# Optimization experiments

Measured on AMD Instinct MI355X. Metric: run time of the kernel, lower is better.

Reference implementation:

```python
import jax, jax.numpy as jnp
import numpy as np

T, L, H, C, D_IN, ED, N, E = 4, 3, 1, 256, 20, 10, 4096, 65536
D = H * C  # 256, pooling width
AH = 4     # pooling attention heads


def setup_inputs() -> dict:
    key = jax.random.key(0)
    ks = jax.random.split(key, 24)
    g = lambda k, s, sc=0.05: jax.random.normal(k, s, jnp.float32) * sc
    return {
        "x": jax.random.normal(ks[0], (N, D_IN), jnp.float32),
        "src": jax.random.randint(ks[1], (E,), 0, N),
        "dst": jax.random.randint(ks[2], (E,), 0, N),
        "edge_attr": jax.random.normal(ks[3], (E, ED), jnp.float32),
        "edge_type": jax.random.randint(ks[4], (E,), 0, T),
        # GATConv params per (edge_type, layer)
        "W0": g(ks[5], (T, D_IN, H * C)),          # layer 0 lin
        "W12": g(ks[6], (T, 2, H * C, H * C)),     # layers 1,2 lin
        "att_src": g(ks[7], (T, L, H, C)),
        "att_dst": g(ks[8], (T, L, H, C)),
        "att_edge": g(ks[9], (T, L, H, C)),
        "lin_edge_w": g(ks[10], (T, L, ED, H * C)),
        "biases": g(ks[11], (T, L, C)),            # H=1 so concat/mean both give C
        "edge_type_weights": jnp.ones((T,), jnp.float32) / T,
        # pooling: MultiheadAttention(D, 4 heads)
        "in_proj_w": g(ks[12], (3 * D, D)),
        "in_proj_b": g(ks[13], (3 * D,)),
        "out_proj_w": g(ks[14], (D, D)),
        "out_proj_b": g(ks[15], (D,)),
        # fusion MLP: 3D -> 2D -> 256
        "fus_w1": g(ks[16], (3 * D, 2 * D)),
        "fus_b1": g(ks[17], (2 * D,)),
        "fus_w2": g(ks[18], (2 * D, 256)),
        "fus_b2": g(ks[19], (256,)),
    }


def _gat(h, src, dst, mask, e_attr, W, a_s, a_d, a_e, We, b, concat):
    # PyG GATConv (edge_dim, add_self_loops=True, fill_value='mean'), eval mode
    Nn = h.shape[0]
    Hh, Cc = a_s.shape
    xl = (h @ W).reshape(Nn, Hh, Cc)
    s_src = jnp.sum(xl * a_s, -1)   # [N,H]
    s_dst = jnp.sum(xl * a_d, -1)   # [N,H]
    s_e = jnp.sum((e_attr @ We).reshape(-1, Hh, Cc) * a_e, -1)  # [E,H]
    # self-loop edge_attr = per-node mean of masked incoming edge_attr
    m = mask.astype(h.dtype)
    cnt = jax.ops.segment_sum(m, dst, Nn)
    loop_attr = jax.ops.segment_sum(e_attr * m[:, None], dst, Nn) / jnp.maximum(cnt, 1.0)[:, None]
    s_loop = jnp.sum((loop_attr @ We).reshape(Nn, Hh, Cc) * a_e, -1)  # [N,H]
    a_real = jax.nn.leaky_relu(s_src[src] + s_dst[dst] + s_e, 0.2)
    a_real = jnp.where(mask[:, None], a_real, -1e30)  # mask edges not of this type
    a_loop = jax.nn.leaky_relu(s_src + s_dst + s_loop, 0.2)
    ar = jnp.arange(Nn)
    idx = jnp.concatenate([dst, ar])    # destination of each (edge + self-loop)
    sidx = jnp.concatenate([src, ar])   # source of each
    scores = jnp.concatenate([a_real, a_loop], 0)  # [E+N, H]
    smax = jax.ops.segment_max(scores, idx, Nn)
    ex = jnp.exp(scores - smax[idx])
    ssum = jax.ops.segment_sum(ex, idx, Nn)
    alpha = ex / (ssum[idx] + 1e-16)
    out = jax.ops.segment_sum(xl[sidx] * alpha[:, :, None], idx, Nn)  # [N,H,C]
    out = out.reshape(Nn, Hh * Cc) if concat else out.mean(1)
    return out + b


def reference(x, src, dst, edge_attr, edge_type, W0, W12, att_src, att_dst,
              att_edge, lin_edge_w, biases, edge_type_weights, in_proj_w,
              in_proj_b, out_proj_w, out_proj_b, fus_w1, fus_b1, fus_w2, fus_b2):
    outs = []
    for t in range(T):
        mask = edge_type == t
        h = x
        for i in range(L):
            W = W0[t] if i == 0 else W12[t, i - 1]
            h = _gat(h, src, dst, mask, edge_attr, W, att_src[t, i],
                     att_dst[t, i], att_edge[t, i], lin_edge_w[t, i],
                     biases[t, i], concat=(i < L - 1))
            h = jax.nn.elu(h)  # dropout off in eval
        outs.append(h)
    w = jax.nn.softmax(edge_type_weights)
    h = sum(w[t] * outs[t] for t in range(T))  # [N, D]
    # HierarchicalGraphPooling
    mean_p = h.mean(0)
    max_p = h.max(0)
    qkv = h @ in_proj_w.T + in_proj_b
    q, k, v = jnp.split(qkv, 3, axis=-1)
    HD = D // AH
    q = q.reshape(-1, AH, HD)
    k = k.reshape(-1, AH, HD)
    v = v.reshape(-1, AH, HD)
    att = jax.nn.softmax(jnp.einsum('nhd,mhd->hnm', q, k) / np.float32(np.sqrt(HD)), axis=-1)
    o = jnp.einsum('hnm,mhd->nhd', att, v).reshape(-1, D) @ out_proj_w.T + out_proj_b
    attn_p = o.mean(0)
    comb = jnp.concatenate([mean_p, max_p, attn_p])  # [3D]
    g = jax.nn.relu(comb @ fus_w1 + fus_b1)
    g = jax.nn.relu(g @ fus_w2 + fus_b2)
    return g[None, :]
```

## Files before the change

### kernel.cpp

```cpp
#include <hip/hip_runtime.h>
#include <math.h>

#define T 4
#define LL 3
#define C 256
#define DIN 20
#define NN 4096
#define EE 65536
#define AHD 4
#define MCH 8
#define QKS 72
#define AST 264
#define SLOTN (16384*64)

#define W_CURSOR 0
#define W_SLSRC  16384
#define F_SLSE   (W_SLSRC + SLOTN)
#define F_XL     (F_SLSE + 3*SLOTN)
#define F_H      (F_XL + T*NN*C/2)
#define F_OPART  F_XL
#define F_SSRC   (F_H + T*NN*C/2)
#define F_SDST   (F_SSRC + T*NN)
#define F_WE     (F_SDST + T*NN)
#define F_HACC   (F_WE + 128)
#define F_WT     (F_HACC + NN*C/2)
#define F_QKV    (F_WT + 768*256/2)
#define F_DPART  (F_QKV + NN*768/2)
#define F_MEANP  (F_DPART + MCH*NN*AHD)
#define F_MAXP   (F_MEANP + C)
#define F_OMEAN  (F_MAXP + C)
#define F_ATTNP  (F_OMEAN + C)
#define F_G1     (F_ATTNP + C)
#define U_W12P   (F_G1 + 512)
#define WS_WORDS (U_W12P + 262144)

static __device__ __forceinline__ float lrelu(float x){ return x > 0.f ? x : 0.2f*x; }
static __device__ __forceinline__ float eluf(float x){ return x > 0.f ? x : __expf(x) - 1.f; }

typedef _Float16 half2_t __attribute__((ext_vector_type(2)));
typedef _Float16 v8h __attribute__((ext_vector_type(8)));
typedef float v4f __attribute__((ext_vector_type(4)));

static __device__ __forceinline__ unsigned pk2(float x, float y){
  half2_t h; h.x = (_Float16)x; h.y = (_Float16)y;
  return __builtin_bit_cast(unsigned, h);
}
static __device__ __forceinline__ unsigned pk2h(_Float16 x, _Float16 y){
  half2_t h; h.x = x; h.y = y;
  return __builtin_bit_cast(unsigned, h);
}
static __device__ __forceinline__ float4 up4(uint2 u){
  half2_t a = __builtin_bit_cast(half2_t, u.x);
  half2_t b = __builtin_bit_cast(half2_t, u.y);
  return make_float4((float)a.x, (float)a.y, (float)b.x, (float)b.y);
}
static __device__ __forceinline__ uint2 dn4(float4 v){
  return make_uint2(pk2(v.x, v.y), pk2(v.z, v.w));
}

static __device__ inline void atomicMaxF(float* addr, float val){
  int* ai = (int*)addr;
  int old = __float_as_int(*addr);
  while (__int_as_float(old) < val){
    int assumed = old;
    old = atomicCAS(ai, assumed, __float_as_int(val));
    if (old == assumed) break;
  }
}

__global__ __launch_bounds__(256) void prep_k(
    const float* __restrict__ x, const float* __restrict__ W0,
    const float* __restrict__ attS, const float* __restrict__ attD,
    _Float16* __restrict__ xlo, float* __restrict__ ssrc, float* __restrict__ sdst,
    const float* __restrict__ w12, _Float16* __restrict__ wpT,
    const float* __restrict__ ipw, _Float16* __restrict__ ip16,
    const float* __restrict__ linE, const float* __restrict__ attE,
    float* we, float* fbase, int* cursor){
  __shared__ float smem[64*65];
  __shared__ float red[64];
  int by = blockIdx.y, bx = blockIdx.x, tid = threadIdx.x;
  if (by < 4){
    int t = by;
    const float* W = W0 + (size_t)t*DIN*C;
    int n0 = bx*8;
    for (int j = 0; j < 8; j++)
      for (int k = tid; k < DIN; k += 256)
        smem[j*DIN + k] = x[(n0+j)*DIN + k];
    __syncthreads();
    float acc[8] = {0,0,0,0,0,0,0,0};
    int c = tid;
    for (int k = 0; k < DIN; k += 4){
      float w0 = W[(k+0)*C + c], w1 = W[(k+1)*C + c], w2 = W[(k+2)*C + c], w3 = W[(k+3)*C + c];
      #pragma unroll
      for (int j = 0; j < 8; j++){
        float4 h4 = *(const float4*)&smem[j*DIN + k];
        acc[j] += w0*h4.x + w1*h4.y + w2*h4.z + w3*h4.w;
      }
    }
    #pragma unroll
    for (int j = 0; j < 8; j++) xlo[((size_t)t*NN + n0 + j)*C + c] = (_Float16)acc[j];
    float aS = attS[t*LL*C + c], aD = attD[t*LL*C + c];
    int lane = c & 63, w = c >> 6;
    #pragma unroll
    for (int j = 0; j < 8; j++){
      float v1 = acc[j]*aS, v2 = acc[j]*aD;
      #pragma unroll
      for (int off = 32; off > 0; off >>= 1){ v1 += __shfl_down(v1, off); v2 += __shfl_down(v2, off); }
      if (lane == 0){ red[j*8 + w] = v1; red[j*8 + 4 + w] = v2; }
    }
    __syncthreads();
    if (c < 16){
      int j = c >> 1, which = c & 1;
      const float* r = red + j*8 + which*4;
      float s = r[0] + r[1] + r[2] + r[3];
      (which ? sdst : ssrc)[t*NN + n0 + j] = s;
    }
  } else if (by < 12){
    if (bx < 16){
      int b8 = by - 4;
      int k0 = (bx >> 2)*64, n0 = (bx & 3)*64;
      const float* src = w12 + ((size_t)b8*256 + k0)*256 + n0;
      int row = tid >> 2, l4 = (tid & 3)*4;
      #pragma unroll
      for (int pass = 0; pass < 4; pass++){
        float4 v = *(const float4*)(src + (size_t)row*256 + pass*16 + l4);
        int o = row*65 + pass*16 + l4;
        smem[o+0] = v.x; smem[o+1] = v.y; smem[o+2] = v.z; smem[o+3] = v.w;
      }
      __syncthreads();
      int n = tid >> 2, seg = tid & 3;
      _Float16* dstp = wpT + ((size_t)b8*256 + n0 + n)*256 + k0 + seg*16;
      v8h h0, h1;
      #pragma unroll
      for (int i = 0; i < 8; i++) h0[i] = (_Float16)smem[(seg*16 + i)*65 + n];
      #pragma unroll
      for (int i = 0; i < 8; i++) h1[i] = (_Float16)smem[(seg*16 + 8 + i)*65 + n];
      *(v8h*)(dstp) = h0;
      *(v8h*)(dstp + 8) = h1;
    }
  } else if (by < 15){
    if (bx < 256){
      int j = (by - 12)*256 + bx;
      ip16[(size_t)j*256 + tid] = (_Float16)ipw[(size_t)j*256 + tid];
    }
  } else {
    if (bx < 12){
      int t = bx / 3, l = bx % 3;
      float ae = attE[(t*LL + l)*C + tid];
      const float* lw = linE + (size_t)((t*LL + l)*10)*C;
      for (int k = 0; k < 10; k++) smem[k*C + tid] = lw[k*C + tid]*ae;
      __syncthreads();
      if (tid < 10){
        float s = 0.f;
        for (int i = 0; i < C; i++) s += smem[tid*C + i];
        we[(t*LL + l)*10 + tid] = s;
      }
    } else if (bx == 12){
      fbase[tid] = 0.f;
      fbase[256 + tid] = -1e30f;
      fbase[512 + tid] = 0.f;
    } else if (bx >= 64 && bx < 128){
      cursor[(bx - 64)*256 + tid] = 0;
    }
  }
}

__global__ __launch_bounds__(256) void scat_k(const int* __restrict__ dst, const int* __restrict__ ety,
                                              const int* __restrict__ srcv, const float* __restrict__ eattr,
                                              const float* __restrict__ we,
                                              int* cursor, int* slot_src, float* slot_se){
  int e = blockIdx.x*256 + threadIdx.x;
  if (e < EE){
    int t = ety[e];
    int gid = dst[e]*T + t;
    int p = atomicAdd(&cursor[gid], 1);
    if (p < 64){
      int sl = gid*64 + p;
      slot_src[sl] = srcv[e];
      float ea[10];
      #pragma unroll
      for (int k = 0; k < 10; k++) ea[k] = eattr[(size_t)e*10 + k];
      #pragma unroll
      for (int l = 0; l < 3; l++){
        const float* w = we + (t*LL + l)*10;
        float s = 0.f;
        #pragma unroll
        for (int k = 0; k < 10; k++) s += ea[k]*w[k];
        slot_se[(size_t)l*SLOTN + sl] = s;
      }
    }
  }
}

__global__ __launch_bounds__(256, 2) void gemm16m_k(const _Float16* __restrict__ hin,
                                                    const _Float16* __restrict__ wpT,
                                                    const float* __restrict__ attS, const float* __restrict__ attD,
                                                    int l, _Float16* __restrict__ xlo,
                                                    float* __restrict__ ssrc, float* __restrict__ sdst){
  __shared__ __align__(16) _Float16 As[64*AST];
  __shared__ float redS[4*64], redD[4*64];
  int t = blockIdx.y;
  int mb = blockIdx.x*64;
  int tid = threadIdx.x;
  int w = tid >> 6, lane = tid & 63;
  int r16 = lane & 15, q = lane >> 4;
  {
    int sr = tid >> 2, sc = (tid & 3)*64;
    const _Float16* hr = hin + ((size_t)(t*NN + mb + sr))*C + sc;
    #pragma unroll
    for (int i = 0; i < 8; i++)
      *(v8h*)(As + (size_t)sr*AST + sc + 8*i) = *(const v8h*)(hr + 8*i);
  }
  __syncthreads();
  int cb = w*64;
  const _Float16* WB = wpT + ((size_t)((t*2 + (l-1))*256 + cb))*256;
  v4f o[4][4];
  #pragma unroll
  for (int i = 0; i < 4; i++)
    #pragma unroll
    for (int j = 0; j < 4; j++) o[i][j] = (v4f){0.f,0.f,0.f,0.f};
  #pragma unroll
  for (int kk = 0; kk < 8; kk++){
    v8h a[4], b[4];
    #pragma unroll
    for (int mi = 0; mi < 4; mi++) a[mi] = *(v8h*)(As + (size_t)(mi*16 + r16)*AST + kk*32 + q*8);
    #pragma unroll
    for (int ni = 0; ni < 4; ni++) b[ni] = *(const v8h*)(WB + (size_t)(ni*16 + r16)*256 + kk*32 + q*8);
    #pragma unroll
    for (int mi = 0; mi < 4; mi++)
      #pragma unroll
      for (int ni = 0; ni < 4; ni++)
        o[mi][ni] = __builtin_amdgcn_mfma_f32_16x16x32_f16(a[mi], b[ni], o[mi][ni], 0, 0, 0);
  }
  int tl = t*LL + l;
  float aS[4], aD[4];
  #pragma unroll
  for (int ni = 0; ni < 4; ni++){
    aS[ni] = attS[tl*C + cb + ni*16 + r16];
    aD[ni] = attD[tl*C + cb + ni*16 + r16];
  }
  #pragma unroll
  for (int mi = 0; mi < 4; mi++)
    #pragma unroll
    for (int rr = 0; rr < 4; rr++){
      int row = mb + mi*16 + q*4 + rr;
      float v1 = 0.f, v2 = 0.f;
      #pragma unroll
      for (int ni = 0; ni < 4; ni++){
        float ov = o[mi][ni][rr];
        xlo[((size_t)t*NN + row)*C + cb + ni*16 + r16] = (_Float16)ov;
        v1 += ov*aS[ni]; v2 += ov*aD[ni];
      }
      v1 += __shfl_xor(v1, 1); v2 += __shfl_xor(v2, 1);
      v1 += __shfl_xor(v1, 2); v2 += __shfl_xor(v2, 2);
      v1 += __shfl_xor(v1, 4); v2 += __shfl_xor(v2, 4);
      v1 += __shfl_xor(v1, 8); v2 += __shfl_xor(v2, 8);
      if (r16 == 0){
        redS[w*64 + mi*16 + q*4 + rr] = v1;
        redD[w*64 + mi*16 + q*4 + rr] = v2;
      }
    }
  __syncthreads();
  if (tid < 64)
    ssrc[t*NN + mb + tid] = redS[tid] + redS[64+tid] + redS[128+tid] + redS[192+tid];
  else if (tid < 128){
    int i = tid - 64;
    sdst[t*NN + mb + i] = redD[i] + redD[64+i] + redD[128+i] + redD[192+i];
  }
}

__global__ __launch_bounds__(256, 2) void qkv16m_k(const _Float16* __restrict__ hacc,
                                                   const _Float16* __restrict__ ip16,
                                                   const float* __restrict__ ipb, _Float16* __restrict__ qkv,
                                                   float* meanp, float* maxp){
  __shared__ __align__(16) _Float16 As[64*AST];
  int p = blockIdx.y;
  int mb = blockIdx.x*64;
  int tid = threadIdx.x;
  int w = tid >> 6, lane = tid & 63;
  int r16 = lane & 15, q = lane >> 4;
  {
    int sr = tid >> 2, sc = (tid & 3)*64;
    const _Float16* hr = hacc + ((size_t)(mb + sr))*C + sc;
    #pragma unroll
    for (int i = 0; i < 8; i++)
      *(v8h*)(As + (size_t)sr*AST + sc + 8*i) = *(const v8h*)(hr + 8*i);
  }
  __syncthreads();
  int cb = p*256 + w*64;
  v4f o[4][4];
  #pragma unroll
  for (int i = 0; i < 4; i++)
    #pragma unroll
    for (int j = 0; j < 4; j++) o[i][j] = (v4f){0.f,0.f,0.f,0.f};
  #pragma unroll
  for (int kk = 0; kk < 8; kk++){
    v8h a[4], b[4];
    #pragma unroll
    for (int mi = 0; mi < 4; mi++) a[mi] = *(v8h*)(As + (size_t)(mi*16 + r16)*AST + kk*32 + q*8);
    #pragma unroll
    for (int ni = 0; ni < 4; ni++) b[ni] = *(const v8h*)(ip16 + (size_t)(cb + ni*16 + r16)*256 + kk*32 + q*8);
    #pragma unroll
    for (int mi = 0; mi < 4; mi++)
      #pragma unroll
      for (int ni = 0; ni < 4; ni++)
        o[mi][ni] = __builtin_amdgcn_mfma_f32_16x16x32_f16(a[mi], b[ni], o[mi][ni], 0, 0, 0);
  }
  float bn[4];
  #pragma unroll
  for (int ni = 0; ni < 4; ni++) bn[ni] = ipb[cb + ni*16 + r16];
  #pragma unroll
  for (int mi = 0; mi < 4; mi++)
    #pragma unroll
    for (int rr = 0; rr < 4; rr++){
      int row = mb + mi*16 + q*4 + rr;
      #pragma unroll
      for (int ni = 0; ni < 4; ni++)
        qkv[(size_t)row*768 + cb + ni*16 + r16] = (_Float16)(o[mi][ni][rr] + bn[ni]);
    }
  if (p == 0){
    float sm = 0.f, mx = -1e30f;
    for (int r = 0; r < 64; r++){
      float v = (float)hacc[(size_t)(mb + r)*C + tid];
      sm += v; mx = fmaxf(mx, v);
    }
    atomicAdd(&meanp[tid], sm*(1.f/4096.f));
    atomicMaxF(&maxp[tid], mx);
  }
}

__global__ __launch_bounds__(256) void agg_k(const _Float16* __restrict__ xl, const float* __restrict__ ssrc,
                                             const float* __restrict__ sdst,
                                             const int* __restrict__ cnt, const int* __restrict__ slot_src,
                                             const float* __restrict__ slot_se,
                                             const float* __restrict__ bias, _Float16* __restrict__ hout,
                                             const float* __restrict__ etw, _Float16* __restrict__ hacc, int l){
  __shared__ float4 sh[4][64];
  int gid = blockIdx.x*4 + (threadIdx.x >> 6);
  int lane = threadIdx.x & 63;
  int n = gid >> 2, t = gid & 3;
  int deg = cnt[gid];
  if (deg > 64) deg = 64;
  float sd = sdst[t*NN + n];
  float se_e = 0.f; int sj = 0;
  if (lane < deg){
    int sl = gid*64 + lane;
    sj = slot_src[sl];
    se_e = slot_se[(size_t)l*SLOTN + sl];
  }
  float ssum_se = se_e;
  #pragma unroll
  for (int o = 32; o > 0; o >>= 1) ssum_se += __shfl_xor(ssum_se, o);
  float sloop = ssum_se / (float)(deg > 0 ? deg : 1);
  float sc = (lane < deg) ? lrelu(ssrc[t*NN + sj] + sd + se_e) : -1e30f;
  float al = lrelu(ssrc[t*NN + n] + sd + sloop);
  float mx = fmaxf(sc, al);
  #pragma unroll
  for (int o = 32; o > 0; o >>= 1) mx = fmaxf(mx, __shfl_xor(mx, o));
  float ex = (lane < deg) ? __expf(sc - mx) : 0.f;
  float ale = __expf(al - mx);
  float ssum = ex;
  #pragma unroll
  for (int o = 32; o > 0; o >>= 1) ssum += __shfl_xor(ssum, o);
  float inv = 1.f/(ssum + ale + 1e-16f);
  const uint2* xl2 = (const uint2*)xl;
  float4 acc = up4(xl2[((size_t)(t*NN + n))*64 + lane]);
  acc.x *= ale; acc.y *= ale; acc.z *= ale; acc.w *= ale;
  int dmax = deg - 1;
  for (int j0 = 0; j0 < deg; j0 += 4){
    float p0 = __shfl(ex, j0);
    float p1 = (j0+1 < deg) ? __shfl(ex, j0+1) : 0.f;
    float p2 = (j0+2 < deg) ? __shfl(ex, j0+2) : 0.f;
    float p3 = (j0+3 < deg) ? __shfl(ex, j0+3) : 0.f;
    int s0 = __shfl(sj, j0);
    int s1 = __shfl(sj, (j0+1 < deg) ? j0+1 : dmax);
    int s2 = __shfl(sj, (j0+2 < deg) ? j0+2 : dmax);
    int s3 = __shfl(sj, (j0+3 < deg) ? j0+3 : dmax);
    float4 v0 = up4(xl2[((size_t)(t*NN + s0))*64 + lane]);
    float4 v1 = up4(xl2[((size_t)(t*NN + s1))*64 + lane]);
    float4 v2 = up4(xl2[((size_t)(t*NN + s2))*64 + lane]);
    float4 v3 = up4(xl2[((size_t)(t*NN + s3))*64 + lane]);
    acc.x += p0*v0.x + p1*v1.x + p2*v2.x + p3*v3.x;
    acc.y += p0*v0.y + p1*v1.y + p2*v2.y + p3*v3.y;
    acc.z += p0*v0.z + p1*v1.z + p2*v2.z + p3*v3.z;
    acc.w += p0*v0.w + p1*v1.w + p2*v2.w + p3*v3.w;
  }
  float4 b4 = *(const float4*)&bias[(t*LL + l)*C + lane*4];
  acc.x = eluf(acc.x*inv + b4.x); acc.y = eluf(acc.y*inv + b4.y);
  acc.z = eluf(acc.z*inv + b4.z); acc.w = eluf(acc.w*inv + b4.w);
  if (l < 2){
    ((uint2*)hout)[((size_t)(t*NN + n))*64 + lane] = dn4(acc);
  } else {
    sh[t][lane] = acc;
    __syncthreads();
    if (t == 0){
      float e0 = etw[0], e1 = etw[1], e2 = etw[2], e3 = etw[3];
      float m = fmaxf(fmaxf(e0,e1), fmaxf(e2,e3));
      float w0 = __expf(e0-m), w1 = __expf(e1-m), w2 = __expf(e2-m), w3 = __expf(e3-m);
      float winv = 1.f/(w0+w1+w2+w3);
      float4 v0 = sh[0][lane], v1 = sh[1][lane], v2 = sh[2][lane], v3 = sh[3][lane];
      float4 s;
      s.x = (w0*v0.x + w1*v1.x + w2*v2.x + w3*v3.x)*winv;
      s.y = (w0*v0.y + w1*v1.y + w2*v2.y + w3*v3.y)*winv;
      s.z = (w0*v0.z + w1*v1.z + w2*v2.z + w3*v3.z)*winv;
      s.w = (w0*v0.w + w1*v1.w + w2*v2.w + w3*v3.w)*winv;
      ((uint2*)hacc)[(size_t)n*64 + lane] = dn4(s);
    }
  }
}

__global__ __launch_bounds__(256, 2) void attn_k(const _Float16* __restrict__ qkv,
                                                 _Float16* __restrict__ opart,
                                                 float* __restrict__ dpart){
  __shared__ __align__(16) _Float16 Ks[64*QKS];
  __shared__ __align__(16) _Float16 VTs[64*QKS];
  __shared__ __align__(16) _Float16 Ps[4][64*QKS];
  int tid = threadIdx.x;
  int wave = tid >> 6, l = tid & 63;
  int nb = blockIdx.x*256 + wave*64;
  int h = blockIdx.y, mc = blockIdx.z;
  int r16 = l & 15, q = l >> 4;
  _Float16* Pw = Ps[wave];

  v8h qf[4][2];
  #pragma unroll
  for (int ni = 0; ni < 4; ni++){
    const _Float16* qrow = qkv + (size_t)(nb + ni*16 + r16)*768 + h*64;
    #pragma unroll
    for (int kk = 0; kk < 2; kk++){
      v8h hv = *(const v8h*)(qrow + kk*32 + q*8);
      #pragma unroll
      for (int i = 0; i < 8; i++) hv[i] = hv[i] * (_Float16)0.125f;
      qf[ni][kk] = hv;
    }
  }

  v4f o[4][4];
  #pragma unroll
  for (int i = 0; i < 4; i++)
    #pragma unroll
    for (int j = 0; j < 4; j++) o[i][j] = (v4f){0.f,0.f,0.f,0.f};
  float dn[4] = {0.f,0.f,0.f,0.f};

  for (int mt = 0; mt < NN/MCH/64; mt++){
    int mb = mc*(NN/MCH) + mt*64;
    __syncthreads();
    {
      int sr = tid >> 2, sc = (tid & 3)*16;
      const _Float16* krow = qkv + (size_t)(mb + sr)*768 + 256 + h*64 + sc;
      *(v8h*)(Ks + (size_t)sr*QKS + sc) = *(const v8h*)(krow);
      *(v8h*)(Ks + (size_t)sr*QKS + sc + 8) = *(const v8h*)(krow + 8);
    }
    {
      int m0 = (tid & 31)*2;
      int db = (tid >> 5)*8;
      const _Float16* v0 = qkv + (size_t)(mb + m0)*768 + 512 + h*64 + db;
      const _Float16* v1 = v0 + 768;
      v8h a = *(const v8h*)v0;
      v8h b = *(const v8h*)v1;
      #pragma unroll
      for (int d = 0; d < 8; d++)
        *(unsigned*)(VTs + (size_t)(db+d)*QKS + m0) = pk2h(a[d], b[d]);
    }
    __syncthreads();
    v4f c[4][4];
    #pragma unroll
    for (int i = 0; i < 4; i++)
      #pragma unroll
      for (int j = 0; j < 4; j++) c[i][j] = (v4f){0.f,0.f,0.f,0.f};
    #pragma unroll
    for (int kk = 0; kk < 2; kk++){
      v8h a[4];
      #pragma unroll
      for (int mi = 0; mi < 4; mi++) a[mi] = *(v8h*)(Ks + (size_t)(mi*16 + r16)*QKS + kk*32 + q*8);
      #pragma unroll
      for (int mi = 0; mi < 4; mi++)
        #pragma unroll
        for (int ni = 0; ni < 4; ni++)
          c[mi][ni] = __builtin_amdgcn_mfma_f32_16x16x32_f16(a[mi], qf[ni][kk], c[mi][ni], 0, 0, 0);
    }
    #pragma unroll
    for (int mi = 0; mi < 4; mi++)
      #pragma unroll
      for (int ni = 0; ni < 4; ni++){
        float e0 = __expf(c[mi][ni][0]), e1 = __expf(c[mi][ni][1]),
              e2 = __expf(c[mi][ni][2]), e3 = __expf(c[mi][ni][3]);
        dn[ni] += e0 + e1 + e2 + e3;
        *(uint2*)(Pw + (size_t)(ni*16 + r16)*QKS + mi*16 + q*4) = make_uint2(pk2(e0,e1), pk2(e2,e3));
      }
    #pragma unroll
    for (int km = 0; km < 2; km++){
      v8h pa[4], vb[4];
      #pragma unroll
      for (int ni = 0; ni < 4; ni++) pa[ni] = *(v8h*)(Pw + (size_t)(ni*16 + r16)*QKS + km*32 + q*8);
      #pragma unroll
      for (int di = 0; di < 4; di++) vb[di] = *(v8h*)(VTs + (size_t)(di*16 + r16)*QKS + km*32 + q*8);
      #pragma unroll
      for (int ni = 0; ni < 4; ni++)
        #pragma unroll
        for (int di = 0; di < 4; di++)
          o[ni][di] = __builtin_amdgcn_mfma_f32_16x16x32_f16(pa[ni], vb[di], o[ni][di], 0, 0, 0);
    }
  }

  _Float16* ob = opart + ((size_t)mc*NN + nb)*C + h*64;
  #pragma unroll
  for (int ni = 0; ni < 4; ni++)
    #pragma unroll
    for (int di = 0; di < 4; di++)
      #pragma unroll
      for (int r = 0; r < 4; r++)
        ob[(size_t)(ni*16 + q*4 + r)*C + di*16 + r16] = (_Float16)o[ni][di][r];
  #pragma unroll
  for (int ni = 0; ni < 4; ni++){
    dn[ni] += __shfl_xor(dn[ni], 16);
    dn[ni] += __shfl_xor(dn[ni], 32);
  }
  if (q == 0){
    #pragma unroll
    for (int ni = 0; ni < 4; ni++)
      dpart[((size_t)mc*NN + nb + ni*16 + r16)*AHD + h] = dn[ni];
  }
}

__global__ __launch_bounds__(256) void attnred_k(const _Float16* __restrict__ opart, const float* __restrict__ dpart,
                                                 float* omean){
  int r0 = blockIdx.x*(NN/256), c = threadIdx.x;
  int head = c >> 6;
  float s = 0.f;
  for (int r = 0; r < NN/256; r++){
    int n = r0 + r;
    float dsum = 0.f, osum = 0.f;
    #pragma unroll
    for (int mc = 0; mc < MCH; mc++){
      dsum += dpart[((size_t)mc*NN + n)*AHD + head];
      osum += (float)opart[((size_t)mc*NN + n)*C + c];
    }
    s += osum / (dsum + 1e-16f);
  }
  atomicAdd(&omean[c], s*(1.f/4096.f));
}

__global__ __launch_bounds__(256) void taila_k(const float* __restrict__ omean, const float* __restrict__ opw,
                                               const float* __restrict__ opb, const float* __restrict__ fb1,
                                               float* attnp, float* g1){
  __shared__ float sh[256];
  int tid = threadIdx.x;
  sh[tid] = omean[tid];
  __syncthreads();
  int jj = tid >> 4, kk = tid & 15;
  int j = blockIdx.x*16 + jj;
  float acc = 0.f;
  #pragma unroll
  for (int i = 0; i < 16; i++){
    int k = kk*16 + i;
    acc += sh[k]*opw[(size_t)j*256 + k];
  }
  acc += __shfl_xor(acc, 1); acc += __shfl_xor(acc, 2);
  acc += __shfl_xor(acc, 4); acc += __shfl_xor(acc, 8);
  if (kk == 0) attnp[j] = acc + opb[j];
  if (blockIdx.x < 2) g1[blockIdx.x*256 + tid] = fb1[blockIdx.x*256 + tid];
}

__global__ __launch_bounds__(512) void tailb_k(const float* __restrict__ meanp, const float* __restrict__ maxp,
                                               const float* __restrict__ attnp, const float* __restrict__ fw1,
                                               float* g1){
  __shared__ float comb[48];
  int b = blockIdx.x, tid = threadIdx.x;
  if (tid < 48){
    int k = b*48 + tid;
    comb[tid] = (k < 256) ? meanp[k] : (k < 512 ? maxp[k-256] : attnp[k-512]);
  }
  __syncthreads();
  float acc = 0.f;
  #pragma unroll 4
  for (int i = 0; i < 48; i++)
    acc += comb[i]*fw1[((size_t)(b*48 + i))*512 + tid];
  atomicAdd(&g1[tid], acc);
}

__global__ __launch_bounds__(256) void tailc_k(const float* __restrict__ g1, const float* __restrict__ fw2,
                                               const float* __restrict__ fb2, float* __restrict__ out){
  __shared__ float g[512];
  __shared__ float red[256];
  int tid = threadIdx.x;
  g[tid] = fmaxf(g1[tid], 0.f);
  g[tid + 256] = fmaxf(g1[tid + 256], 0.f);
  __syncthreads();
  int j = blockIdx.x*32 + (tid & 31);
  int kp = tid >> 5;
  float acc = 0.f;
  #pragma unroll 4
  for (int i = 0; i < 64; i++){
    int k = kp*64 + i;
    acc += g[k]*fw2[(size_t)k*256 + j];
  }
  red[tid] = acc;
  __syncthreads();
  if (tid < 32){
    float s = 0.f;
    #pragma unroll
    for (int p = 0; p < 8; p++) s += red[p*32 + tid];
    out[j] = fmaxf(s + fb2[j], 0.f);
  }
}

extern "C" void kernel_launch(void* const* d_in, const int* in_sizes, int n_in,
                              void* d_out, int out_size, void* d_ws, size_t ws_size,
                              hipStream_t stream){
  const float* x     = (const float*)d_in[0];
  const int*   srcv  = (const int*)d_in[1];
  const int*   dstv  = (const int*)d_in[2];
  const float* eattr = (const float*)d_in[3];
  const int*   etyp  = (const int*)d_in[4];
  const float* W0    = (const float*)d_in[5];
  const float* W12   = (const float*)d_in[6];
  const float* attS  = (const float*)d_in[7];
  const float* attD  = (const float*)d_in[8];
  const float* attE  = (const float*)d_in[9];
  const float* linE  = (const float*)d_in[10];
  const float* bias  = (const float*)d_in[11];
  const float* etw   = (const float*)d_in[12];
  const float* ipw   = (const float*)d_in[13];
  const float* ipb   = (const float*)d_in[14];
  const float* opw   = (const float*)d_in[15];
  const float* opb   = (const float*)d_in[16];
  const float* fw1   = (const float*)d_in[17];
  const float* fb1   = (const float*)d_in[18];
  const float* fw2   = (const float*)d_in[19];
  const float* fb2   = (const float*)d_in[20];
  float* out = (float*)d_out;

  if (ws_size < (size_t)WS_WORDS*4) return;

  int*       ip    = (int*)d_ws;
  float*     fp    = (float*)d_ws;
  _Float16*  xl16  = (_Float16*)(fp + F_XL);
  _Float16*  h16   = (_Float16*)(fp + F_H);
  _Float16*  op16  = (_Float16*)(fp + F_OPART);
  _Float16*  hacc16= (_Float16*)(fp + F_HACC);
  _Float16*  ip16  = (_Float16*)(fp + F_WT);
  _Float16*  qkv16 = (_Float16*)(fp + F_QKV);
  _Float16*  wpT   = (_Float16*)(fp + U_W12P);

  prep_k<<<dim3(512, 16), 256, 0, stream>>>(x, W0, attS, attD,
                                            xl16, fp + F_SSRC, fp + F_SDST,
                                            W12, wpT, ipw, ip16, linE, attE,
                                            fp + F_WE, fp + F_MEANP, ip + W_CURSOR);

  scat_k<<<EE/256, 256, 0, stream>>>(dstv, etyp, srcv, eattr, fp + F_WE,
                                     ip + W_CURSOR, ip + W_SLSRC, fp + F_SLSE);

  agg_k<<<(NN*T)/4, 256, 0, stream>>>(xl16, fp + F_SSRC, fp + F_SDST,
                                      ip + W_CURSOR, ip + W_SLSRC, fp + F_SLSE,
                                      bias, h16, etw, hacc16, 0);
  for (int l = 1; l < 3; l++){
    gemm16m_k<<<dim3(NN/64, T), 256, 0, stream>>>(h16, wpT, attS, attD, l,
                                                  xl16, fp + F_SSRC, fp + F_SDST);
    agg_k<<<(NN*T)/4, 256, 0, stream>>>(xl16, fp + F_SSRC, fp + F_SDST,
                                        ip + W_CURSOR, ip + W_SLSRC, fp + F_SLSE,
                                        bias, h16, etw, hacc16, l);
  }

  qkv16m_k<<<dim3(NN/64, 3), 256, 0, stream>>>(hacc16, ip16, ipb, qkv16,
                                               fp + F_MEANP, fp + F_MAXP);
  attn_k<<<dim3(NN/256, AHD, MCH), 256, 0, stream>>>(qkv16, op16, fp + F_DPART);

  attnred_k<<<256, 256, 0, stream>>>(op16, fp + F_DPART, fp + F_OMEAN);
  taila_k<<<16, 256, 0, stream>>>(fp + F_OMEAN, opw, opb, fb1, fp + F_ATTNP, fp + F_G1);
  tailb_k<<<16, 512, 0, stream>>>(fp + F_MEANP, fp + F_MAXP, fp + F_ATTNP, fw1, fp + F_G1);
  tailc_k<<<8, 256, 0, stream>>>(fp + F_G1, fw2, fb2, out);
}
```

Before: 268.3 us.

## Drop LDS staging in MFMA GEMMs and fuse tail kernels with partial sums

The two MFMA GEMM kernels now read their A operand straight from global memory instead of staging a 64-row tile in LDS behind a barrier. This cuts the LDS footprint and the sync, but the same A rows are now re-read from global/L2 by all four waves. The taila and tailb tail kernels are merged into one kernel that computes the out-proj rows inline for the chunks that need them. The atomicAdd accumulation into g1 is replaced by per-block partial sums that tailc reduces together with the bias, removing one launch and the atomics.

```diff
diff --git a/kernel.cpp b/kernel.cpp
--- a/kernel.cpp
+++ b/kernel.cpp
@@ -10,7 +10,6 @@
 #define AHD 4
 #define MCH 8
 #define QKS 72
-#define AST 264
 #define SLOTN (16384*64)
 
 #define W_CURSOR 0
@@ -29,9 +28,8 @@
 #define F_MEANP  (F_DPART + MCH*NN*AHD)
 #define F_MAXP   (F_MEANP + C)
 #define F_OMEAN  (F_MAXP + C)
-#define F_ATTNP  (F_OMEAN + C)
-#define F_G1     (F_ATTNP + C)
-#define U_W12P   (F_G1 + 512)
+#define F_PART   (F_OMEAN + C)
+#define U_W12P   (F_PART + 16*512)
 #define WS_WORDS (U_W12P + 262144)
 
 static __device__ __forceinline__ float lrelu(float x){ return x > 0.f ? x : 0.2f*x; }
@@ -197,21 +195,13 @@
                                                     const float* __restrict__ attS, const float* __restrict__ attD,
                                                     int l, _Float16* __restrict__ xlo,
                                                     float* __restrict__ ssrc, float* __restrict__ sdst){
-  __shared__ __align__(16) _Float16 As[64*AST];
   __shared__ float redS[4*64], redD[4*64];
   int t = blockIdx.y;
   int mb = blockIdx.x*64;
   int tid = threadIdx.x;
   int w = tid >> 6, lane = tid & 63;
   int r16 = lane & 15, q = lane >> 4;
-  {
-    int sr = tid >> 2, sc = (tid & 3)*64;
-    const _Float16* hr = hin + ((size_t)(t*NN + mb + sr))*C + sc;
-    #pragma unroll
-    for (int i = 0; i < 8; i++)
-      *(v8h*)(As + (size_t)sr*AST + sc + 8*i) = *(const v8h*)(hr + 8*i);
-  }
-  __syncthreads();
+  const _Float16* HA = hin + ((size_t)(t*NN + mb))*C;
   int cb = w*64;
   const _Float16* WB = wpT + ((size_t)((t*2 + (l-1))*256 + cb))*256;
   v4f o[4][4];
@@ -223,7 +213,7 @@
   for (int kk = 0; kk < 8; kk++){
     v8h a[4], b[4];
     #pragma unroll
-    for (int mi = 0; mi < 4; mi++) a[mi] = *(v8h*)(As + (size_t)(mi*16 + r16)*AST + kk*32 + q*8);
+    for (int mi = 0; mi < 4; mi++) a[mi] = *(const v8h*)(HA + (size_t)(mi*16 + r16)*C + kk*32 + q*8);
     #pragma unroll
     for (int ni = 0; ni < 4; ni++) b[ni] = *(const v8h*)(WB + (size_t)(ni*16 + r16)*256 + kk*32 + q*8);
     #pragma unroll
@@ -273,20 +263,12 @@
                                                    const _Float16* __restrict__ ip16,
                                                    const float* __restrict__ ipb, _Float16* __restrict__ qkv,
                                                    float* meanp, float* maxp){
-  __shared__ __align__(16) _Float16 As[64*AST];
   int p = blockIdx.y;
   int mb = blockIdx.x*64;
   int tid = threadIdx.x;
   int w = tid >> 6, lane = tid & 63;
   int r16 = lane & 15, q = lane >> 4;
-  {
-    int sr = tid >> 2, sc = (tid & 3)*64;
-    const _Float16* hr = hacc + ((size_t)(mb + sr))*C + sc;
-    #pragma unroll
-    for (int i = 0; i < 8; i++)
-      *(v8h*)(As + (size_t)sr*AST + sc + 8*i) = *(const v8h*)(hr + 8*i);
-  }
-  __syncthreads();
+  const _Float16* HA = hacc + (size_t)mb*C;
   int cb = p*256 + w*64;
   v4f o[4][4];
   #pragma unroll
@@ -297,7 +279,7 @@
   for (int kk = 0; kk < 8; kk++){
     v8h a[4], b[4];
     #pragma unroll
-    for (int mi = 0; mi < 4; mi++) a[mi] = *(v8h*)(As + (size_t)(mi*16 + r16)*AST + kk*32 + q*8);
+    for (int mi = 0; mi < 4; mi++) a[mi] = *(const v8h*)(HA + (size_t)(mi*16 + r16)*C + kk*32 + q*8);
     #pragma unroll
     for (int ni = 0; ni < 4; ni++) b[ni] = *(const v8h*)(ip16 + (size_t)(cb + ni*16 + r16)*256 + kk*32 + q*8);
     #pragma unroll
@@ -541,51 +523,51 @@
   atomicAdd(&omean[c], s*(1.f/4096.f));
 }
 
-__global__ __launch_bounds__(256) void taila_k(const float* __restrict__ omean, const float* __restrict__ opw,
-                                               const float* __restrict__ opb, const float* __restrict__ fb1,
-                                               float* attnp, float* g1){
-  __shared__ float sh[256];
-  int tid = threadIdx.x;
-  sh[tid] = omean[tid];
-  __syncthreads();
-  int jj = tid >> 4, kk = tid & 15;
-  int j = blockIdx.x*16 + jj;
-  float acc = 0.f;
-  #pragma unroll
-  for (int i = 0; i < 16; i++){
-    int k = kk*16 + i;
-    acc += sh[k]*opw[(size_t)j*256 + k];
-  }
-  acc += __shfl_xor(acc, 1); acc += __shfl_xor(acc, 2);
-  acc += __shfl_xor(acc, 4); acc += __shfl_xor(acc, 8);
-  if (kk == 0) attnp[j] = acc + opb[j];
-  if (blockIdx.x < 2) g1[blockIdx.x*256 + tid] = fb1[blockIdx.x*256 + tid];
-}
-
-__global__ __launch_bounds__(512) void tailb_k(const float* __restrict__ meanp, const float* __restrict__ maxp,
-                                               const float* __restrict__ attnp, const float* __restrict__ fw1,
-                                               float* g1){
+__global__ __launch_bounds__(512) void tailab_k(const float* __restrict__ omean, const float* __restrict__ opw,
+                                                const float* __restrict__ opb,
+                                                const float* __restrict__ meanp, const float* __restrict__ maxp,
+                                                const float* __restrict__ fw1, float* __restrict__ part){
+  __shared__ float om[256];
   __shared__ float comb[48];
   int b = blockIdx.x, tid = threadIdx.x;
+  if (tid < 256) om[tid] = omean[tid];
+  __syncthreads();
   if (tid < 48){
     int k = b*48 + tid;
-    comb[tid] = (k < 256) ? meanp[k] : (k < 512 ? maxp[k-256] : attnp[k-512]);
+    float v;
+    if (k < 256) v = meanp[k];
+    else if (k < 512) v = maxp[k-256];
+    else {
+      int j = k - 512;
+      float acc = 0.f;
+      #pragma unroll 4
+      for (int i = 0; i < 256; i++) acc += om[i]*opw[(size_t)j*256 + i];
+      v = acc + opb[j];
+    }
+    comb[tid] = v;
   }
   __syncthreads();
   float acc = 0.f;
   #pragma unroll 4
   for (int i = 0; i < 48; i++)
     acc += comb[i]*fw1[((size_t)(b*48 + i))*512 + tid];
-  atomicAdd(&g1[tid], acc);
-}
-
-__global__ __launch_bounds__(256) void tailc_k(const float* __restrict__ g1, const float* __restrict__ fw2,
-                                               const float* __restrict__ fb2, float* __restrict__ out){
+  part[(size_t)b*512 + tid] = acc;
+}
+
+__global__ __launch_bounds__(256) void tailc_k(const float* __restrict__ part, const float* __restrict__ fb1,
+                                               const float* __restrict__ fw2, const float* __restrict__ fb2,
+                                               float* __restrict__ out){
   __shared__ float g[512];
   __shared__ float red[256];
   int tid = threadIdx.x;
-  g[tid] = fmaxf(g1[tid], 0.f);
-  g[tid + 256] = fmaxf(g1[tid + 256], 0.f);
+  float s0 = fb1[tid], s1 = fb1[tid + 256];
+  #pragma unroll
+  for (int b = 0; b < 16; b++){
+    s0 += part[(size_t)b*512 + tid];
+    s1 += part[(size_t)b*512 + tid + 256];
+  }
+  g[tid] = fmaxf(s0, 0.f);
+  g[tid + 256] = fmaxf(s1, 0.f);
   __syncthreads();
   int j = blockIdx.x*32 + (tid & 31);
   int kp = tid >> 5;
@@ -667,7 +649,7 @@
   attn_k<<<dim3(NN/256, AHD, MCH), 256, 0, stream>>>(qkv16, op16, fp + F_DPART);
 
   attnred_k<<<256, 256, 0, stream>>>(op16, fp + F_DPART, fp + F_OMEAN);
-  taila_k<<<16, 256, 0, stream>>>(fp + F_OMEAN, opw, opb, fb1, fp + F_ATTNP, fp + F_G1);
-  tailb_k<<<16, 512, 0, stream>>>(fp + F_MEANP, fp + F_MAXP, fp + F_ATTNP, fw1, fp + F_G1);
-  tailc_k<<<8, 256, 0, stream>>>(fp + F_G1, fw2, fb2, out);
-}
+  tailab_k<<<16, 512, 0, stream>>>(fp + F_OMEAN, opw, opb,
+                                   fp + F_MEANP, fp + F_MAXP, fw1, fp + F_PART);
+  tailc_k<<<8, 256, 0, stream>>>(fp + F_PART, fb1, fw2, fb2, out);
+}
```

Result: slower. 277.6 us (+3.5%).
